# Kernel optimization log

Hardware: AMD Instinct MI355X
Metric: run time of the kernel (lower is better)

## Reference

```python
import jax, jax.numpy as jnp
import numpy as np

B, N, C = 2, 2048, 1024
H = 8
DH = C // H  # head dim = 128


def setup_inputs() -> dict:
    key = jax.random.key(0)
    ks = jax.random.split(key, 10)
    s = 1.0 / np.sqrt(C)
    return {
        "inputs_q": jax.random.normal(ks[0], (B, N, C), dtype=jnp.float32),
        "inputs_kv": jax.random.normal(ks[1], (B, N, C), dtype=jnp.float32),
        "Wq": jax.random.normal(ks[2], (C, C), dtype=jnp.float32) * s,
        "bq": jnp.zeros((C,), dtype=jnp.float32),
        "Wk": jax.random.normal(ks[3], (C, C), dtype=jnp.float32) * s,
        "bk": jnp.zeros((C,), dtype=jnp.float32),
        "Wv": jax.random.normal(ks[4], (C, C), dtype=jnp.float32) * s,
        "bv": jnp.zeros((C,), dtype=jnp.float32),
        "Wo": jax.random.normal(ks[5], (C, C), dtype=jnp.float32) * s,
        "bo": jnp.zeros((C,), dtype=jnp.float32),
    }


def reference(inputs_q, inputs_kv, Wq, bq, Wk, bk, Wv, bv, Wo, bo):
    # QKV linear projections
    q = inputs_q @ Wq + bq           # [B, N, C]
    k = inputs_kv @ Wk + bk          # [B, M, C]
    v = inputs_kv @ Wv + bv          # [B, M, C]
    # split heads
    q = q.reshape(B, N, H, DH)
    k = k.reshape(B, -1, H, DH)
    v = v.reshape(B, -1, H, DH)
    # explicit attention, matching attend(): scale by 1/sqrt(head_dim)
    attn = jnp.einsum('bnhc,bmhc->bhnm', q, k) * (1.0 / np.sqrt(DH))
    normalized = jax.nn.softmax(attn, axis=-1)  # f32 softmax (inputs are f32)
    summed = jnp.einsum('bhnm,bmhd->bnhd', normalized, v)
    summed = summed.reshape(B, N, C)  # merge heads: ...n(hd)
    # output linear
    return summed @ Wo + bo
```

## Files before the change

### kernel.cpp

```cpp
#include <hip/hip_runtime.h>

typedef unsigned short u16;
typedef __bf16 bf16;
typedef __attribute__((ext_vector_type(8))) __bf16 bf16x8;
typedef __attribute__((ext_vector_type(4))) float f32x4;
typedef __attribute__((ext_vector_type(16))) float f32x16;

#define AS1(p) ((const __attribute__((address_space(1))) void*)(p))
#define AS3(p) ((__attribute__((address_space(3))) void*)(p))

__device__ __forceinline__ u16 f2bf(float f) {
  unsigned u = __builtin_bit_cast(unsigned, f);
  u += 0x7fffu + ((u >> 16) & 1u);
  return (u16)(u >> 16);
}

static constexpr int  B_ = 2, N_ = 2048, C_ = 1024, H_ = 8, DH_ = 128;
static constexpr long SZ_IN = (long)B_ * N_ * C_;
static constexpr long SZ_W  = (long)C_ * C_;

__global__ void k_cast(const float* __restrict__ q, const float* __restrict__ kv,
                       const float* __restrict__ W0, const float* __restrict__ W1,
                       const float* __restrict__ W2, const float* __restrict__ W3,
                       u16* __restrict__ qb, u16* __restrict__ kvb,
                       u16* __restrict__ WT)
{
  __shared__ u16 t[64][65];
  int tid = threadIdx.x;
  if (blockIdx.y < 2) {
    const float* src = blockIdx.y ? kv : q;
    u16* dst = blockIdx.y ? kvb : qb;
    long i = ((long)blockIdx.x * 256 + tid) * 8;
    float4 a = *(const float4*)(src + i);
    float4 b = *(const float4*)(src + i + 4);
    uint4 v;
    v.x = f2bf(a.x) | ((unsigned)f2bf(a.y) << 16);
    v.y = f2bf(a.z) | ((unsigned)f2bf(a.w) << 16);
    v.z = f2bf(b.x) | ((unsigned)f2bf(b.y) << 16);
    v.w = f2bf(b.z) | ((unsigned)f2bf(b.w) << 16);
    *(uint4*)(dst + i) = v;
    return;
  }
  int x = blockIdx.x;
  if (x >= 1024) return;
  int z = x >> 8, tile = x & 255;
  const float* W = (z == 0) ? W0 : (z == 1) ? W1 : (z == 2) ? W2 : W3;
  u16* dst = WT + (long)z * SZ_W;
  int n0 = (tile & 15) * 64, k0 = (tile >> 4) * 64;
#pragma unroll
  for (int r = 0; r < 4; ++r) {
    int slot = r * 256 + tid;
    int row = slot >> 4, c4 = slot & 15;
    float4 a = *(const float4*)(W + (long)(k0 + row) * 1024 + n0 + c4 * 4);
    t[c4*4+0][row] = f2bf(a.x);
    t[c4*4+1][row] = f2bf(a.y);
    t[c4*4+2][row] = f2bf(a.z);
    t[c4*4+3][row] = f2bf(a.w);
  }
  __syncthreads();
#pragma unroll
  for (int r = 0; r < 4; ++r) {
    int slot = r * 256 + tid;
    int row = slot >> 4, c4 = slot & 15;
    uint2 v;
    v.x = t[row][c4*4+0] | ((unsigned)t[row][c4*4+1] << 16);
    v.y = t[row][c4*4+2] | ((unsigned)t[row][c4*4+3] << 16);
    *(uint2*)(dst + (long)(n0 + row) * 1024 + k0 + c4 * 4) = v;
  }
}

__device__ __forceinline__ void gemm_main_128x128(
    const u16* __restrict__ A, const u16* __restrict__ BT,
    u16* lA, u16* lB, int m0, int n0, int tid, f32x4 acc[4][4])
{
  int w = tid >> 6, l = tid & 63, quad = l >> 4, lm = l & 15;
  int wm = w >> 1, wn = w & 1;
  int srow = tid >> 2, schunk = tid & 3;
  int sxw = (srow >> 1) & 3;
  int sxr = (lm >> 1) & 3;
  const u16* Ag = A + (long)(m0 + srow) * 1024 + (schunk ^ sxw) * 8;
  const u16* Bg = BT + (long)(n0 + srow) * 1024 + (schunk ^ sxw) * 8;
  u16* lAw = lA + w * 512;
  u16* lBw = lB + w * 512;
  for (int kb = 0; kb < 32; ++kb) {
    const u16* Agk = Ag + kb * 32;
    const u16* Bgk = Bg + kb * 32;
    __builtin_amdgcn_global_load_lds(AS1(Agk),           AS3(lAw),        16, 0, 0);
    __builtin_amdgcn_global_load_lds(AS1(Agk + 64*1024), AS3(lAw + 2048), 16, 0, 0);
    __builtin_amdgcn_global_load_lds(AS1(Bgk),           AS3(lBw),        16, 0, 0);
    __builtin_amdgcn_global_load_lds(AS1(Bgk + 64*1024), AS3(lBw + 2048), 16, 0, 0);
    __syncthreads();
    bf16x8 af[4], bfr[4];
#pragma unroll
    for (int mi = 0; mi < 4; ++mi)
      af[mi] = *(const bf16x8*)(lA + (wm*64 + mi*16 + lm)*32 + ((quad ^ sxr))*8);
#pragma unroll
    for (int ni = 0; ni < 4; ++ni)
      bfr[ni] = *(const bf16x8*)(lB + (wn*64 + ni*16 + lm)*32 + ((quad ^ sxr))*8);
#pragma unroll
    for (int mi = 0; mi < 4; ++mi)
#pragma unroll
      for (int ni = 0; ni < 4; ++ni)
        acc[mi][ni] = __builtin_amdgcn_mfma_f32_16x16x32_bf16(af[mi], bfr[ni], acc[mi][ni], 0, 0, 0);
    __syncthreads();
  }
}

__global__ __launch_bounds__(256, 3)
void k_gemm_qkv(const u16* __restrict__ qb, const u16* __restrict__ kvb,
                const u16* __restrict__ wt,
                const float* __restrict__ bq, const float* __restrict__ bk,
                const float* __restrict__ bv,
                u16* __restrict__ Qb, u16* __restrict__ Kb, u16* __restrict__ VTb)
{
  __shared__ u16 lA[4096], lB[4096];
  int tid = threadIdx.x;
  int z = blockIdx.z;
  f32x4 acc[4][4] = {};
  int w = tid >> 6, l = tid & 63, quad = l >> 4, lm = l & 15;
  int wm = w >> 1, wn = w & 1;

  if (z == 2) {
    int m0 = blockIdx.y * 128, n0 = blockIdx.x * 128;
    gemm_main_128x128(kvb, wt + 2 * SZ_W, lA, lB, m0, n0, tid, acc);
#pragma unroll
    for (int ni = 0; ni < 4; ++ni) {
      int n = n0 + wn*64 + ni*16 + lm;
      float bb = bv[n];
      int h = n >> 7, dd = n & 127;
#pragma unroll
      for (int mi = 0; mi < 4; ++mi) {
        int mbase = m0 + wm*64 + mi*16 + quad*4;
        int bidx = mbase >> 11, nn = mbase & 2047;
        u16 o0 = f2bf(acc[mi][ni][0] + bb), o1 = f2bf(acc[mi][ni][1] + bb);
        u16 o2 = f2bf(acc[mi][ni][2] + bb), o3 = f2bf(acc[mi][ni][3] + bb);
        uint2 v; v.x = o0 | ((unsigned)o1 << 16); v.y = o2 | ((unsigned)o3 << 16);
        *(uint2*)(VTb + ((long)(bidx*8 + h)*128 + dd)*2048 + nn) = v;
      }
    }
  } else {
    const u16* X = (z == 0) ? qb : kvb;
    const float* bias = (z == 0) ? bq : bk;
    u16* dst = (z == 0) ? Qb : Kb;
    float scale = (z == 0) ? 0.08838834764831845f : 1.0f;
    int m0 = blockIdx.x * 128, n0 = blockIdx.y * 128;
    gemm_main_128x128(wt + (long)z * SZ_W, X, lA, lB, m0, n0, tid, acc);
#pragma unroll
    for (int mi = 0; mi < 4; ++mi) {
      int chb = m0 + wm*64 + mi*16 + quad*4;
      int h = chb >> 7, d = chb & 127;
      float4 bb = *(const float4*)(bias + chb);
#pragma unroll
      for (int ni = 0; ni < 4; ++ni) {
        int tok = n0 + wn*64 + ni*16 + lm;
        int bidx = tok >> 11, nn = tok & 2047;
        u16 o0 = f2bf((acc[mi][ni][0] + bb.x) * scale);
        u16 o1 = f2bf((acc[mi][ni][1] + bb.y) * scale);
        u16 o2 = f2bf((acc[mi][ni][2] + bb.z) * scale);
        u16 o3 = f2bf((acc[mi][ni][3] + bb.w) * scale);
        uint2 v; v.x = o0 | ((unsigned)o1 << 16); v.y = o2 | ((unsigned)o3 << 16);
        *(uint2*)(dst + ((long)(bidx*8 + h)*2048 + nn)*128 + d) = v;
      }
    }
  }
}

__global__ __launch_bounds__(512, 2)
void k_attn(const u16* __restrict__ Qb, const u16* __restrict__ Kb,
            const u16* __restrict__ VTb, u16* __restrict__ Sout)
{
  __shared__ u16 smem[43520];
  u16*   lP    = smem + 32768;
  float* lStat = (float*)(smem + 43008);

  int tid = threadIdx.x;
  int w = tid >> 6, l = tid & 63;
  int l5 = l >> 5, c31 = l & 31;
  int qg = w >> 1, kh = w & 1;
  int bh = blockIdx.x;
  int q0 = blockIdx.y * 128 + qg * 32;
  const u16* Qg = Qb + ((long)bh * 2048 + q0) * 128;
  const u16* Kg = Kb + (long)bh * 2048 * 128;
  const u16* Vg = VTb + (long)bh * 128 * 2048;
  u16* lPw = lP + w * 1280;

  bf16x8 qf[8];
#pragma unroll
  for (int c = 0; c < 8; ++c)
    qf[c] = *(const bf16x8*)(Qg + (long)c31 * 128 + c*16 + l5*8);

  f32x16 accO[4] = {};
  float sumP[16] = {};

  auto stage = [&](int tt) {
    int bufK = (tt & 1) * 8192;
    int bufV = 16384 + (tt & 1) * 8192;
#pragma unroll
    for (int j = 0; j < 2; ++j) {
      int s = j*512 + tid;
      int r = s >> 4, sl = s & 15;
      __builtin_amdgcn_global_load_lds(
          AS1(Kg + (long)(tt*64 + r)*128 + ((sl ^ (r & 15)) * 8)),
          AS3(smem + bufK + (j*512 + w*64)*8), 16, 0, 0);
    }
#pragma unroll
    for (int j = 0; j < 2; ++j) {
      int s = j*512 + tid;
      int d = s >> 3, sl = s & 7;
      __builtin_amdgcn_global_load_lds(
          AS1(Vg + (long)d*2048 + tt*64 + ((sl ^ (d & 7)) * 8)),
          AS3(smem + bufV + (j*512 + w*64)*8), 16, 0, 0);
    }
  };

  stage(0);

#pragma unroll 1
  for (int t = 0; t < 32; ++t) {
    __syncthreads();
    if (t < 31) stage(t + 1);

    const u16* bK = smem + (t & 1) * 8192;
    const u16* bV = smem + 16384 + (t & 1) * 8192;

    f32x16 accS[2] = {};
#pragma unroll
    for (int c = 0; c < 8; ++c) {
      int r = kh*32 + c31;
      bf16x8 kf = *(const bf16x8*)(bK + (r*16 + ((2*c + l5) ^ (l & 15)))*8);
      accS[c & 1] = __builtin_amdgcn_mfma_f32_32x32x16_bf16(qf[c], kf, accS[c & 1], 0, 0, 0);
    }

#pragma unroll
    for (int g = 0; g < 16; ++g) {
      int R = (g & 3) + 8*(g >> 2) + 4*l5;
      float p = __expf(accS[0][g] + accS[1][g]);
      sumP[g] += p;
      lPw[R*40 + c31] = f2bf(p);
    }

#pragma unroll
    for (int ks = 0; ks < 2; ++ks) {
      bf16x8 pf = *(const bf16x8*)(lPw + c31*40 + ks*16 + l5*8);
#pragma unroll
      for (int dt = 0; dt < 4; ++dt) {
        int d = dt*32 + c31;
        int cc = kh*4 + ks*2 + l5;
        bf16x8 vf = *(const bf16x8*)(bV + (d*8 + (cc ^ (d & 7)))*8);
        accO[dt] = __builtin_amdgcn_mfma_f32_32x32x16_bf16(pf, vf, accO[dt], 0, 0, 0);
      }
    }
  }

#pragma unroll
  for (int g = 0; g < 16; ++g) {
    float s = sumP[g];
    s += __shfl_xor(s, 1);
    s += __shfl_xor(s, 2);
    s += __shfl_xor(s, 4);
    s += __shfl_xor(s, 8);
    s += __shfl_xor(s, 16);
    sumP[g] = s;
    int R = (g & 3) + 8*(g >> 2) + 4*l5;
    lStat[(qg*2 + kh)*32 + R] = s;
  }

  float* lO = (float*)smem;
  __syncthreads();
  if (kh == 1) {
#pragma unroll
    for (int dt = 0; dt < 4; ++dt)
#pragma unroll
      for (int g = 0; g < 16; ++g) {
        int R = (g & 3) + 8*(g >> 2) + 4*l5;
        lO[(qg*32 + R)*128 + dt*32 + c31] = accO[dt][g];
      }
  }
  __syncthreads();
  if (kh == 0) {
    int b = bh >> 3, h = bh & 7;
#pragma unroll
    for (int g = 0; g < 16; ++g) {
      int R = (g & 3) + 8*(g >> 2) + 4*l5;
      float linv = 1.f / (lStat[(qg*2)*32 + R] + lStat[(qg*2 + 1)*32 + R]);
#pragma unroll
      for (int dt = 0; dt < 4; ++dt) {
        float v = (accO[dt][g] + lO[(qg*32 + R)*128 + dt*32 + c31]) * linv;
        Sout[((long)(b*2048 + q0 + R))*1024 + h*128 + dt*32 + c31] = f2bf(v);
      }
    }
  }
}

__global__ __launch_bounds__(256, 3)
void k_gemm_out(const u16* __restrict__ S, const u16* __restrict__ WoT,
                const float* __restrict__ bo, float* __restrict__ out)
{
  __shared__ u16 lA[4096], lB[4096];
  int tid = threadIdx.x;
  int m0 = blockIdx.x * 128, n0 = blockIdx.y * 128;
  f32x4 acc[4][4] = {};
  gemm_main_128x128(WoT, S, lA, lB, m0, n0, tid, acc);

  int w = tid >> 6, l = tid & 63, quad = l >> 4, lm = l & 15;
  int wm = w >> 1, wn = w & 1;
#pragma unroll
  for (int mi = 0; mi < 4; ++mi) {
    int chb = m0 + wm*64 + mi*16 + quad*4;
    float4 bb = *(const float4*)(bo + chb);
#pragma unroll
    for (int ni = 0; ni < 4; ++ni) {
      int tok = n0 + wn*64 + ni*16 + lm;
      float4 v;
      v.x = acc[mi][ni][0] + bb.x;
      v.y = acc[mi][ni][1] + bb.y;
      v.z = acc[mi][ni][2] + bb.z;
      v.w = acc[mi][ni][3] + bb.w;
      *(float4*)(out + (long)tok * 1024 + chb) = v;
    }
  }
}

extern "C" void kernel_launch(void* const* d_in, const int* in_sizes, int n_in,
                              void* d_out, int out_size, void* d_ws, size_t ws_size,
                              hipStream_t stream)
{
  const float* inq  = (const float*)d_in[0];
  const float* inkv = (const float*)d_in[1];
  const float* Wq = (const float*)d_in[2];
  const float* bq = (const float*)d_in[3];
  const float* Wk = (const float*)d_in[4];
  const float* bk = (const float*)d_in[5];
  const float* Wv = (const float*)d_in[6];
  const float* bv = (const float*)d_in[7];
  const float* Wo = (const float*)d_in[8];
  const float* bo = (const float*)d_in[9];

  u16* ws   = (u16*)d_ws;
  u16* ABUF = ws;
  u16* KVB  = ws + SZ_IN;
  u16* WT   = ws + 2 * SZ_IN;
  u16* Qb   = WT + 4 * SZ_W;
  u16* Kb   = Qb + SZ_IN;
  u16* VTb  = Kb + SZ_IN;

  k_cast    <<<dim3(2048, 3),   256, 0, stream>>>(inq, inkv, Wq, Wk, Wv, Wo, ABUF, KVB, WT);
  k_gemm_qkv<<<dim3(8, 32, 3),  256, 0, stream>>>(ABUF, KVB, WT, bq, bk, bv, Qb, Kb, VTb);
  k_attn    <<<dim3(16, 16),    512, 0, stream>>>(Qb, Kb, VTb, ABUF);
  k_gemm_out<<<dim3(8, 32),     256, 0, stream>>>(ABUF, WT + 3 * SZ_W, bo, (float*)d_out);
}
```

Before: 214.9 us.

## Keep softmax P in registers via transposed S MFMA and lane shuffles

Swaps the MFMA operand order so the score tile is computed transposed (keys x queries). Each lane then holds consecutive key values for one query and can pack them directly into the bf16 A-operand of the PV MFMA. A single cross-half lane shuffle replaces the per-iteration LDS write and read of P. Row sums become one scalar per lane with one final shuffle, and the LDS footprint shrinks, which removes LDS traffic and scalar bf16 stores at the cost of register shuffles and selects.

```diff
diff --git a/kernel.cpp b/kernel.cpp
--- a/kernel.cpp
+++ b/kernel.cpp
@@ -13,6 +13,12 @@
   unsigned u = __builtin_bit_cast(unsigned, f);
   u += 0x7fffu + ((u >> 16) & 1u);
   return (u16)(u >> 16);
+}
+
+__device__ __forceinline__ unsigned pkbf(float a, float b) {
+  unsigned lo = (unsigned)__builtin_bit_cast(unsigned short, (__bf16)a);
+  unsigned hi = (unsigned)__builtin_bit_cast(unsigned short, (__bf16)b);
+  return lo | (hi << 16);
 }
 
 static constexpr int  B_ = 2, N_ = 2048, C_ = 1024, H_ = 8, DH_ = 128;
@@ -169,9 +175,8 @@
 void k_attn(const u16* __restrict__ Qb, const u16* __restrict__ Kb,
             const u16* __restrict__ VTb, u16* __restrict__ Sout)
 {
-  __shared__ u16 smem[43520];
-  u16*   lP    = smem + 32768;
-  float* lStat = (float*)(smem + 43008);
+  __shared__ u16 smem[33280];
+  float* lStat = (float*)(smem + 32768);
 
   int tid = threadIdx.x;
   int w = tid >> 6, l = tid & 63;
@@ -182,7 +187,6 @@
   const u16* Qg = Qb + ((long)bh * 2048 + q0) * 128;
   const u16* Kg = Kb + (long)bh * 2048 * 128;
   const u16* Vg = VTb + (long)bh * 128 * 2048;
-  u16* lPw = lP + w * 1280;
 
   bf16x8 qf[8];
 #pragma unroll
@@ -190,7 +194,7 @@
     qf[c] = *(const bf16x8*)(Qg + (long)c31 * 128 + c*16 + l5*8);
 
   f32x16 accO[4] = {};
-  float sumP[16] = {};
+  float sumP = 0.f;
 
   auto stage = [&](int tt) {
     int bufK = (tt & 1) * 8192;
@@ -228,41 +232,58 @@
     for (int c = 0; c < 8; ++c) {
       int r = kh*32 + c31;
       bf16x8 kf = *(const bf16x8*)(bK + (r*16 + ((2*c + l5) ^ (l & 15)))*8);
-      accS[c & 1] = __builtin_amdgcn_mfma_f32_32x32x16_bf16(qf[c], kf, accS[c & 1], 0, 0, 0);
-    }
-
-#pragma unroll
-    for (int g = 0; g < 16; ++g) {
-      int R = (g & 3) + 8*(g >> 2) + 4*l5;
-      float p = __expf(accS[0][g] + accS[1][g]);
-      sumP[g] += p;
-      lPw[R*40 + c31] = f2bf(p);
+      accS[c & 1] = __builtin_amdgcn_mfma_f32_32x32x16_bf16(kf, qf[c], accS[c & 1], 0, 0, 0);
+    }
+
+    unsigned own0[2], own1[2], own2[2], own3[2];
+    {
+      float ss = 0.f;
+#pragma unroll
+      for (int G = 0; G < 4; ++G) {
+        float p0 = __expf(accS[0][4*G+0] + accS[1][4*G+0]);
+        float p1 = __expf(accS[0][4*G+1] + accS[1][4*G+1]);
+        float p2 = __expf(accS[0][4*G+2] + accS[1][4*G+2]);
+        float p3 = __expf(accS[0][4*G+3] + accS[1][4*G+3]);
+        ss += (p0 + p1) + (p2 + p3);
+        unsigned wa = pkbf(p0, p1), wb = pkbf(p2, p3);
+        if (G == 0) { own0[0] = wa; own0[1] = wb; }
+        if (G == 1) { own1[0] = wa; own1[1] = wb; }
+        if (G == 2) { own2[0] = wa; own2[1] = wb; }
+        if (G == 3) { own3[0] = wa; own3[1] = wb; }
+      }
+      sumP += ss;
     }
 
 #pragma unroll
     for (int ks = 0; ks < 2; ++ks) {
-      bf16x8 pf = *(const bf16x8*)(lPw + c31*40 + ks*16 + l5*8);
+      unsigned xa, xb;
+      if (ks == 0) { xa = l5 ? own0[0] : own1[0]; xb = l5 ? own0[1] : own1[1]; }
+      else         { xa = l5 ? own2[0] : own3[0]; xb = l5 ? own2[1] : own3[1]; }
+      unsigned ra = __shfl_xor((int)xa, 32);
+      unsigned rb = __shfl_xor((int)xb, 32);
+      uint4 uw;
+      if (ks == 0) {
+        uw.x = l5 ? ra : own0[0];  uw.y = l5 ? rb : own0[1];
+        uw.z = l5 ? own1[0] : ra;  uw.w = l5 ? own1[1] : rb;
+      } else {
+        uw.x = l5 ? ra : own2[0];  uw.y = l5 ? rb : own2[1];
+        uw.z = l5 ? own3[0] : ra;  uw.w = l5 ? own3[1] : rb;
+      }
+      bf16x8 pa = __builtin_bit_cast(bf16x8, uw);
 #pragma unroll
       for (int dt = 0; dt < 4; ++dt) {
         int d = dt*32 + c31;
         int cc = kh*4 + ks*2 + l5;
         bf16x8 vf = *(const bf16x8*)(bV + (d*8 + (cc ^ (d & 7)))*8);
-        accO[dt] = __builtin_amdgcn_mfma_f32_32x32x16_bf16(pf, vf, accO[dt], 0, 0, 0);
-      }
-    }
-  }
-
-#pragma unroll
-  for (int g = 0; g < 16; ++g) {
-    float s = sumP[g];
-    s += __shfl_xor(s, 1);
-    s += __shfl_xor(s, 2);
-    s += __shfl_xor(s, 4);
-    s += __shfl_xor(s, 8);
-    s += __shfl_xor(s, 16);
-    sumP[g] = s;
-    int R = (g & 3) + 8*(g >> 2) + 4*l5;
-    lStat[(qg*2 + kh)*32 + R] = s;
+        accO[dt] = __builtin_amdgcn_mfma_f32_32x32x16_bf16(pa, vf, accO[dt], 0, 0, 0);
+      }
+    }
+  }
+
+  {
+    float s = sumP;
+    s += __shfl_xor(s, 32);
+    lStat[(qg*2 + kh)*32 + c31] = s;
   }
 
   float* lO = (float*)smem;
```

Result: no change. 212.5 us (-1.1%).
